# Kernel tuning notes

Hardware: AMD Instinct MI355X
Metric: run time of the kernel (lower is better)

Reference implementation:

```python
import math
import jax, jax.numpy as jnp
import numpy as np

NUM_HEADS = 16
TAU_RCS, LAMBDA_RCS = 2.0, 0.6
PATCH = 16
PREFIX = 8
GAUSS_STD = 5.0


def gaussian_window(d1, d2, std):
    c = 1.0 / (std * math.sqrt(2.0))
    k1 = (jnp.arange(d1, dtype=jnp.float32) - (d1 - 1) / 2.0) * c
    k2 = (jnp.arange(d2, dtype=jnp.float32) - (d2 - 1) / 2.0) * c
    return jnp.exp(-(k1[:, None] ** 2 + k2[None, :] ** 2))  # [d1, d2]


def attention_addition(d1, d2, prefix, std):
    # out[(a,b),(c,d)] = window[a-c+d1-1, b-d+d2-1]  (conv of delta images with window)
    win = gaussian_window(2 * d1 - 1, 2 * d2 - 1, std)
    ia = jnp.arange(d1)
    jb = jnp.arange(d2)
    r = ia[:, None] - ia[None, :] + (d1 - 1)   # [d1, d1]
    s = jb[:, None] - jb[None, :] + (d2 - 1)   # [d2, d2]
    add = win[r[:, None, :, None], s[None, :, None, :]]  # [d1,d2,d1,d2]
    add = add.reshape(d1 * d2, d1 * d2)
    add = jnp.pad(add, ((prefix, 0), (prefix, 0)))  # zero rows/cols for prefix tokens
    return add[None]  # [1, N, N]


def setup_inputs() -> dict:
    key = jax.random.key(0)
    ks = jax.random.split(key, 5)
    B, C = 4, 1024
    d1 = d2 = 512 // PATCH  # 32
    N = d1 * d2 + PREFIX    # 1032
    H = NUM_HEADS
    x = jax.random.normal(ks[0], (B, N, C), dtype=jnp.float32)
    qkv_w = jax.random.normal(ks[1], (3 * C, C), dtype=jnp.float32) * 0.02
    qkv_b = jnp.zeros((3 * C,), dtype=jnp.float32)
    proj_w = jax.random.normal(ks[2], (C, C), dtype=jnp.float32) * 0.02
    proj_b = jnp.zeros((C,), dtype=jnp.float32)
    attn_add = attention_addition(d1, d2, PREFIX, GAUSS_STD)
    # stored RCS attention maps are softmax outputs -> row-normalized positives
    rcs = jax.random.uniform(ks[3], (B * H, N, N), dtype=jnp.float32)
    rcs = rcs / jnp.sum(rcs, axis=-1, keepdims=True)
    return {"x": x, "qkv_w": qkv_w, "qkv_b": qkv_b, "proj_w": proj_w,
            "proj_b": proj_b, "attn_addition": attn_add, "rcs_attn": rcs}


def reference(x, qkv_w, qkv_b, proj_w, proj_b, attn_addition, rcs_attn):
    B, N, C = x.shape
    H = NUM_HEADS
    hd = C // H
    scale = hd ** -0.5
    qkv = jnp.einsum('bnc,dc->bnd', x, qkv_w) + qkv_b  # [B,N,3C]
    q, k, v = jnp.split(qkv, 3, axis=-1)
    def to_heads(t):
        return t.reshape(B, N, H, hd).transpose(0, 2, 1, 3).reshape(B * H, N, hd)
    k = to_heads(k)
    v = to_heads(v)
    # custom K-K attention with additive Gaussian bias
    attn = jnp.einsum('bnd,bmd->bnm', k, k) * scale + attn_addition
    attn = jax.nn.softmax(attn, axis=-1)
    # RCS blending with stored intermediate attention maps
    attn = TAU_RCS * ((1.0 - LAMBDA_RCS) * attn + LAMBDA_RCS * rcs_attn)
    out = jnp.einsum('bnm,bmd->bnd', attn, v)  # [B*H, N, hd]
    out = out.reshape(B, H, N, hd).transpose(0, 2, 1, 3).reshape(B, N, C)
    out = jnp.einsum('bnc,dc->bnd', out, proj_w) + proj_b
    return out
```

## Files before the change

kernel.cpp:

```cpp
#include <hip/hip_runtime.h>
#include <stdint.h>

#define NSEQ 1032
#define CDIM 1024
#define HD 64
#define H_HEADS 16
#define BROWS 4128
#define SCALE 0.125f

typedef __attribute__((ext_vector_type(8))) short bf16x8;
typedef __attribute__((ext_vector_type(4))) float f32x4;

__device__ __forceinline__ unsigned short f2bf(float f) {
  union { float f; uint32_t u; } c; c.f = f;
  uint32_t u = c.u;
  return (unsigned short)((u + 0x7fffu + ((u >> 16) & 1u)) >> 16);
}

__device__ __forceinline__ void gl16(const void* gp, void* lp) {
  __builtin_amdgcn_global_load_lds((const __attribute__((address_space(1))) void*)gp,
                                   (__attribute__((address_space(3))) void*)lp, 16, 0, 0);
}

__global__ void convert_f32_bf16(const float* __restrict__ src, unsigned short* __restrict__ dst, int n4) {
  int i = blockIdx.x * blockDim.x + threadIdx.x;
  if (i >= n4) return;
  float4 v = ((const float4*)src)[i];
  ushort4 o;
  o.x = f2bf(v.x); o.y = f2bf(v.y); o.z = f2bf(v.z); o.w = f2bf(v.w);
  ((ushort4*)dst)[i] = o;
}

template<int MODE>
__global__ __launch_bounds__(256, 2) void gemm_bt(
    const unsigned short* __restrict__ A,
    const unsigned short* __restrict__ Bw,
    const float* __restrict__ bias,
    unsigned short* __restrict__ outK,
    unsigned short* __restrict__ outV,
    float* __restrict__ outF,
    int M, int K)
{
  __shared__ unsigned short As[128 * 32];
  __shared__ unsigned short Bs[128 * 32];
  const int t = threadIdx.x;
  const int w = t >> 6, lane = t & 63, lr = lane & 15, lg = lane >> 4;
  const int wr = w >> 1, wc = w & 1;
  const int m0 = blockIdx.y * 128, n0 = blockIdx.x * 128;
  f32x4 acc[4][4] = {};

  for (int ks = 0; ks < K; ks += 32) {
    #pragma unroll
    for (int q = 0; q < 2; ++q) {
      const int o = t + (q << 8);
      const int row = o >> 2, kc = o & 3;
      int ra = m0 + row; ra = ra < M ? ra : M - 1;
      gl16(A + (size_t)ra * K + ks + kc * 8, (void*)(As + o * 8));
      gl16(Bw + (size_t)(n0 + row) * K + ks + kc * 8, (void*)(Bs + o * 8));
    }
    __syncthreads();
    bf16x8 af[4], bfr[4];
    #pragma unroll
    for (int m = 0; m < 4; ++m)
      af[m] = *(const bf16x8*)(As + (wr * 64 + m * 16 + lr) * 32 + lg * 8);
    #pragma unroll
    for (int n = 0; n < 4; ++n)
      bfr[n] = *(const bf16x8*)(Bs + (wc * 64 + n * 16 + lr) * 32 + lg * 8);
    #pragma unroll
    for (int m = 0; m < 4; ++m)
      #pragma unroll
      for (int n = 0; n < 4; ++n)
        acc[m][n] = __builtin_amdgcn_mfma_f32_16x16x32_bf16(af[m], bfr[n], acc[m][n], 0, 0, 0);
    __syncthreads();
  }

  #pragma unroll
  for (int m = 0; m < 4; ++m) {
    const int rowb = m0 + wr * 64 + m * 16 + lg * 4;
    #pragma unroll
    for (int n = 0; n < 4; ++n) {
      const int col = n0 + wc * 64 + n * 16 + lr;
      const float bv = bias[col];
      #pragma unroll
      for (int r = 0; r < 4; ++r) {
        const int row = rowb + r;
        if (row >= M) continue;
        const float v = acc[m][n][r] + bv;
        if (MODE == 0) {
          const int b = row / NSEQ, nn = row - b * NSEQ;
          if (col < CDIM) {
            const int h = col >> 6, d = col & 63;
            outK[((size_t)(b * H_HEADS + h) * NSEQ + nn) * HD + d] = f2bf(v);
          } else {
            const int jj = col - CDIM, h = jj >> 6, d = jj & 63;
            outV[((size_t)(b * H_HEADS + h) * HD + d) * NSEQ + nn] = f2bf(v);
          }
        } else {
          outF[(size_t)row * CDIM + col] = v;
        }
      }
    }
  }
}

__global__ __launch_bounds__(256, 2) void attn_fused(
    const unsigned short* __restrict__ Kb,
    const unsigned short* __restrict__ Vt,
    const float* __restrict__ rcs,
    unsigned short* __restrict__ outp)
{
  __shared__ __align__(16) unsigned short Kc[2][64 * 64];
  __shared__ __align__(16) unsigned short Vs[2][64 * 64];
  __shared__ __align__(16) float As[2][64 * 64];
  __shared__ unsigned short Ps[64 * 72];
  const int t = threadIdx.x;
  const int w = t >> 6, lane = t & 63, lr = lane & 15, lg = lane >> 4;
  const int bid = blockIdx.x;
  const int nb = (bid & 7) * 136 + (bid >> 3);
  const int bh = nb / 17, rt = nb - bh * 17;
  const int i_base = rt * 64 + w * 16;
  const int arow = w * 16 + lr;
  const float* rbase = rcs + (size_t)bh * NSEQ * NSEQ;
  const unsigned short* kbase = Kb + (size_t)bh * NSEQ * HD;
  const unsigned short* vbase = Vt + (size_t)bh * HD * NSEQ;

  auto stage = [&](int tile, int buf) {
    const int tB = tile * 64;
    #pragma unroll
    for (int q = 0; q < 2; ++q) {
      const int p = t + (q << 8);
      const int row = p >> 3, sch = p & 7;
      const int gch = (sch ^ row) & 7;
      int mrow = tB + row; if (mrow > NSEQ - 1) mrow = NSEQ - 1;
      gl16(kbase + (size_t)mrow * HD + gch * 8, (void*)(Kc[buf] + p * 8));
    }
    #pragma unroll
    for (int q = 0; q < 2; ++q) {
      const int p = t + (q << 8);
      const int row = p >> 3, sch = p & 7;
      const int gch = (sch ^ row) & 7;
      int gc = tB + gch * 8; if (gc > NSEQ - 8) gc = NSEQ - 8;
      gl16(vbase + (size_t)row * NSEQ + gc, (void*)(Vs[buf] + p * 8));
    }
    #pragma unroll
    for (int q = 0; q < 4; ++q) {
      const int p = t + (q << 8);
      const int row = p >> 4, sch = p & 15;
      const int gch = (sch & 8) | ((sch ^ row) & 7);
      int grow = rt * 64 + row; if (grow > NSEQ - 1) grow = NSEQ - 1;
      int gcol = tB + gch * 4; if (gcol > NSEQ - 4) gcol = NSEQ - 4;
      gl16(rbase + (size_t)grow * NSEQ + gcol, (void*)(As[buf] + p * 4));
    }
  };

  bf16x8 akr[2];
  {
    int row = i_base + lr; if (row > NSEQ - 1) row = NSEQ - 1;
    const unsigned short* p = kbase + (size_t)row * HD + lg * 8;
    akr[0] = *(const bf16x8*)(p);
    akr[1] = *(const bf16x8*)(p + 32);
  }

  const int irow_base = i_base + lg * 4;
  int i1v[4], j1v[4]; float iokf[4];
  #pragma unroll
  for (int r = 0; r < 4; ++r) {
    const int irow = irow_base + r;
    const int ip = irow - 8;
    i1v[r] = ip >> 5; j1v[r] = ip & 31;
    iokf[r] = (irow >= 8) ? 1.f : 0.f;
  }

  f32x4 accP[4] = {};
  f32x4 accR[4] = {};
  float lsum[4] = {0.f, 0.f, 0.f, 0.f};

  stage(0, 0);

  for (int mt = 0; mt < 17; ++mt) {
    const int mB = mt * 64;
    const int cur = mt & 1, nxt = cur ^ 1;

    if (mt < 16) {
      stage(mt + 1, nxt);
      asm volatile("s_waitcnt vmcnt(8)");
    } else {
      asm volatile("s_waitcnt vmcnt(0)");
    }
    __builtin_amdgcn_sched_barrier(0);
    __builtin_amdgcn_s_barrier();
    __builtin_amdgcn_sched_barrier(0);

    const unsigned short* kc = Kc[cur];
    const unsigned short* vsb = Vs[cur];

    f32x4 s[4];
    #pragma unroll
    for (int fn = 0; fn < 4; ++fn) {
      const int row = 16 * fn + lr;
      const int r7 = row & 7;
      f32x4 z = {0.f, 0.f, 0.f, 0.f};
      bf16x8 b0 = *(const bf16x8*)(kc + row * 64 + ((lg ^ r7) & 7) * 8);
      bf16x8 b1 = *(const bf16x8*)(kc + row * 64 + (((4 + lg) ^ r7) & 7) * 8);
      z = __builtin_amdgcn_mfma_f32_16x16x32_bf16(akr[0], b0, z, 0, 0, 0);
      z = __builtin_amdgcn_mfma_f32_16x16x32_bf16(akr[1], b1, z, 0, 0, 0);
      s[fn] = z;
    }

    #pragma unroll
    for (int fn = 0; fn < 4; ++fn) {
      const int mcol = mB + 16 * fn + lr;
      const int mp = mcol - 8;
      const int m1 = mp >> 5, m2 = mp & 31;
      const float mokf = (mcol >= 8 && mcol < NSEQ) ? 1.f : 0.f;
      const bool mlt = (mcol < NSEQ);
      #pragma unroll
      for (int r = 0; r < 4; ++r) {
        const int di = i1v[r] - m1, dj = j1v[r] - m2;
        const float ad = __expf(-0.02f * (float)(di * di + dj * dj)) * iokf[r] * mokf;
        const float sv = s[fn][r] * SCALE + ad;
        const float p = mlt ? __expf(sv) : 0.f;
        lsum[r] += p;
        Ps[(w * 16 + lg * 4 + r) * 72 + 16 * fn + lr] = f2bf(p);
      }
    }

    bf16x8 af[2];
    #pragma unroll
    for (int kf = 0; kf < 2; ++kf) {
      bf16x8 a;
      const int kg = mB + kf * 32 + lg * 8;
      if (kg + 8 <= NSEQ) {
        const float* ab = As[cur] + arow * 64;
        const int c0 = kf * 8 + 2 * lg;
        const int s0 = (c0 & 8) | ((c0 ^ arow) & 7);
        const int s1 = (c0 & 8) | (((c0 + 1) ^ arow) & 7);
        f32x4 lo = *(const f32x4*)(ab + s0 * 4);
        f32x4 hi = *(const f32x4*)(ab + s1 * 4);
        a[0] = (short)f2bf(lo[0]); a[1] = (short)f2bf(lo[1]);
        a[2] = (short)f2bf(lo[2]); a[3] = (short)f2bf(lo[3]);
        a[4] = (short)f2bf(hi[0]); a[5] = (short)f2bf(hi[1]);
        a[6] = (short)f2bf(hi[2]); a[7] = (short)f2bf(hi[3]);
      } else {
        #pragma unroll
        for (int j = 0; j < 8; ++j) a[j] = 0;
      }
      af[kf] = a;
    }

    bf16x8 pa0 = *(const bf16x8*)(Ps + (w * 16 + lr) * 72 + lg * 8);
    bf16x8 pa1 = *(const bf16x8*)(Ps + (w * 16 + lr) * 72 + 32 + lg * 8);
    #pragma unroll
    for (int fd = 0; fd < 4; ++fd) {
      const int row = 16 * fd + lr;
      const int r7 = row & 7;
      bf16x8 v0 = *(const bf16x8*)(vsb + row * 64 + ((lg ^ r7) & 7) * 8);
      bf16x8 v1 = *(const bf16x8*)(vsb + row * 64 + (((4 + lg) ^ r7) & 7) * 8);
      accP[fd] = __builtin_amdgcn_mfma_f32_16x16x32_bf16(pa0, v0, accP[fd], 0, 0, 0);
      accP[fd] = __builtin_amdgcn_mfma_f32_16x16x32_bf16(pa1, v1, accP[fd], 0, 0, 0);
      accR[fd] = __builtin_amdgcn_mfma_f32_16x16x32_bf16(af[0], v0, accR[fd], 0, 0, 0);
      accR[fd] = __builtin_amdgcn_mfma_f32_16x16x32_bf16(af[1], v1, accR[fd], 0, 0, 0);
    }

    __builtin_amdgcn_sched_barrier(0);
    __builtin_amdgcn_s_barrier();
    __builtin_amdgcn_sched_barrier(0);
  }

  #pragma unroll
  for (int r = 0; r < 4; ++r) {
    float v = lsum[r];
    v += __shfl_xor(v, 1); v += __shfl_xor(v, 2);
    v += __shfl_xor(v, 4); v += __shfl_xor(v, 8);
    lsum[r] = v;
  }

  const int b = bh >> 4, hh = bh & 15;
  #pragma unroll
  for (int fd = 0; fd < 4; ++fd) {
    #pragma unroll
    for (int r = 0; r < 4; ++r) {
      const int irow = i_base + lg * 4 + r;
      if (irow < NSEQ) {
        const float val = 0.8f * accP[fd][r] / lsum[r] + 1.2f * accR[fd][r];
        outp[(size_t)(b * NSEQ + irow) * CDIM + hh * 64 + 16 * fd + lr] = f2bf(val);
      }
    }
  }
}

extern "C" void kernel_launch(void* const* d_in, const int* in_sizes, int n_in,
                              void* d_out, int out_size, void* d_ws, size_t ws_size,
                              hipStream_t stream) {
  (void)in_sizes; (void)n_in; (void)out_size; (void)ws_size;
  const float* x      = (const float*)d_in[0];
  const float* qkv_w  = (const float*)d_in[1];
  const float* qkv_b  = (const float*)d_in[2];
  const float* proj_w = (const float*)d_in[3];
  const float* proj_b = (const float*)d_in[4];
  const float* rcs    = (const float*)d_in[6];
  float* out = (float*)d_out;

  char* ws = (char*)d_ws;
  unsigned short* x_bf = (unsigned short*)ws; ws += (size_t)BROWS * CDIM * 2;
  unsigned short* wkv  = (unsigned short*)ws; ws += (size_t)2048 * CDIM * 2;
  unsigned short* wp   = (unsigned short*)ws; ws += (size_t)1024 * CDIM * 2;
  unsigned short* Kb   = (unsigned short*)ws; ws += (size_t)64 * NSEQ * HD * 2;
  unsigned short* Vt   = (unsigned short*)ws; ws += (size_t)64 * HD * NSEQ * 2;
  unsigned short* op   = (unsigned short*)ws; ws += (size_t)BROWS * CDIM * 2;

  const int n1 = BROWS * CDIM / 4, n2 = 2048 * CDIM / 4, n3 = 1024 * CDIM / 4;
  convert_f32_bf16<<<(n1 + 255) / 256, 256, 0, stream>>>(x, x_bf, n1);
  convert_f32_bf16<<<(n2 + 255) / 256, 256, 0, stream>>>(qkv_w + 1024 * 1024, wkv, n2);
  convert_f32_bf16<<<(n3 + 255) / 256, 256, 0, stream>>>(proj_w, wp, n3);

  gemm_bt<0><<<dim3(16, 33), 256, 0, stream>>>(x_bf, wkv, qkv_b + 1024, Kb, Vt, nullptr, BROWS, CDIM);
  attn_fused<<<1088, 256, 0, stream>>>(Kb, Vt, rcs, op);
  gemm_bt<1><<<dim3(8, 33), 256, 0, stream>>>(op, wp, proj_b, nullptr, nullptr, out, BROWS, CDIM);
}
```

Before: 199.0 us.

## Replace per-element Gaussian exp with recurrence, precompute staging addresses, restructure barriers

Replaces the per-tile exp evaluation of the Gaussian bias with a multiplicative recurrence across m-tiles: each step multiplies u by v*C1 and v by C2, exploiting that advancing the tile by 64 columns shifts di by 2. Staging source and destination addresses are precomputed once, so non-tail tiles skip clamping arithmetic, and only the last tile keeps the clamped path. The wait-then-barrier moves to the end of each iteration, and s_setprio is raised around the MFMA blocks. Over 17 steps the recurrence can build up rounding error in the bias, and the vmcnt(0) wait at the end of each iteration may give up some of the load overlap the previous vmcnt(8) scheme allowed.

```diff
diff --git a/kernel.cpp b/kernel.cpp
--- a/kernel.cpp
+++ b/kernel.cpp
@@ -124,8 +124,36 @@
   const unsigned short* kbase = Kb + (size_t)bh * NSEQ * HD;
   const unsigned short* vbase = Vt + (size_t)bh * HD * NSEQ;
 
-  auto stage = [&](int tile, int buf) {
-    const int tB = tile * 64;
+  const unsigned short* srck[2]; int dok[2];
+  const unsigned short* srcv[2]; int dov[2];
+  const float* srca[4]; int doa[4];
+  #pragma unroll
+  for (int q = 0; q < 2; ++q) {
+    const int p = t + (q << 8);
+    const int row = p >> 3, sch = p & 7;
+    const int gch = (sch ^ row) & 7;
+    srck[q] = kbase + (size_t)row * HD + gch * 8;  dok[q] = p * 8;
+    srcv[q] = vbase + (size_t)row * NSEQ + gch * 8; dov[q] = p * 8;
+  }
+  #pragma unroll
+  for (int q = 0; q < 4; ++q) {
+    const int p = t + (q << 8);
+    const int row = p >> 4, sch = p & 15;
+    const int gch = (sch & 8) | ((sch ^ row) & 7);
+    int grow = rt * 64 + row; if (grow > NSEQ - 1) grow = NSEQ - 1;
+    srca[q] = rbase + (size_t)grow * NSEQ + gch * 4;  doa[q] = p * 4;
+  }
+
+  auto stage_fast = [&](int tB, int buf) {
+    #pragma unroll
+    for (int q = 0; q < 2; ++q) gl16(srck[q] + (size_t)tB * HD, (void*)(Kc[buf] + dok[q]));
+    #pragma unroll
+    for (int q = 0; q < 2; ++q) gl16(srcv[q] + tB, (void*)(Vs[buf] + dov[q]));
+    #pragma unroll
+    for (int q = 0; q < 4; ++q) gl16(srca[q] + tB, (void*)(As[buf] + doa[q]));
+  };
+  auto stage_tail = [&](int buf) {
+    const int tB = 1024;
     #pragma unroll
     for (int q = 0; q < 2; ++q) {
       const int p = t + (q << 8);
@@ -162,38 +190,48 @@
   }
 
   const int irow_base = i_base + lg * 4;
-  int i1v[4], j1v[4]; float iokf[4];
-  #pragma unroll
-  for (int r = 0; r < 4; ++r) {
-    const int irow = irow_base + r;
-    const int ip = irow - 8;
-    i1v[r] = ip >> 5; j1v[r] = ip & 31;
-    iokf[r] = (irow >= 8) ? 1.f : 0.f;
-  }
+  float u[16], v[16];
+  {
+    #pragma unroll
+    for (int fn = 0; fn < 4; ++fn) {
+      const int x = 16 * fn + lr;
+      const int m1_0 = ((x + 24) >> 5) - 1;
+      const int m2 = (x - 8) & 31;
+      #pragma unroll
+      for (int r = 0; r < 4; ++r) {
+        const int irow = irow_base + r;
+        const int ip = irow - 8;
+        const int i1 = ip >> 5, j1 = ip & 31;
+        const int di = i1 - m1_0, dj = j1 - m2;
+        const float iok = (irow >= 8) ? 1.f : 0.f;
+        u[fn * 4 + r] = __expf(-0.02f * (float)(di * di + dj * dj)) * iok;
+        v[fn * 4 + r] = __expf(0.08f * (float)di);
+      }
+    }
+  }
+  const float C1 = 0.92311634639f;
+  const float C2 = 0.85214378896f;
 
   f32x4 accP[4] = {};
   f32x4 accR[4] = {};
   float lsum[4] = {0.f, 0.f, 0.f, 0.f};
 
-  stage(0, 0);
+  stage_fast(0, 0);
+  asm volatile("s_waitcnt vmcnt(0)");
+  __builtin_amdgcn_s_barrier();
+  __builtin_amdgcn_sched_barrier(0);
 
   for (int mt = 0; mt < 17; ++mt) {
     const int mB = mt * 64;
     const int cur = mt & 1, nxt = cur ^ 1;
 
-    if (mt < 16) {
-      stage(mt + 1, nxt);
-      asm volatile("s_waitcnt vmcnt(8)");
-    } else {
-      asm volatile("s_waitcnt vmcnt(0)");
-    }
-    __builtin_amdgcn_sched_barrier(0);
-    __builtin_amdgcn_s_barrier();
-    __builtin_amdgcn_sched_barrier(0);
+    if (mt < 15)      stage_fast(mB + 64, nxt);
+    else if (mt == 15) stage_tail(nxt);
 
     const unsigned short* kc = Kc[cur];
     const unsigned short* vsb = Vs[cur];
 
+    __builtin_amdgcn_s_setprio(1);
     f32x4 s[4];
     #pragma unroll
     for (int fn = 0; fn < 4; ++fn) {
@@ -206,22 +244,22 @@
       z = __builtin_amdgcn_mfma_f32_16x16x32_bf16(akr[1], b1, z, 0, 0, 0);
       s[fn] = z;
     }
+    __builtin_amdgcn_s_setprio(0);
 
     #pragma unroll
     for (int fn = 0; fn < 4; ++fn) {
       const int mcol = mB + 16 * fn + lr;
-      const int mp = mcol - 8;
-      const int m1 = mp >> 5, m2 = mp & 31;
-      const float mokf = (mcol >= 8 && mcol < NSEQ) ? 1.f : 0.f;
+      const float mok = (mcol >= 8 && mcol < NSEQ) ? 1.f : 0.f;
       const bool mlt = (mcol < NSEQ);
       #pragma unroll
       for (int r = 0; r < 4; ++r) {
-        const int di = i1v[r] - m1, dj = j1v[r] - m2;
-        const float ad = __expf(-0.02f * (float)(di * di + dj * dj)) * iokf[r] * mokf;
-        const float sv = s[fn][r] * SCALE + ad;
+        const int fi = fn * 4 + r;
+        const float sv = s[fn][r] * SCALE + u[fi] * mok;
         const float p = mlt ? __expf(sv) : 0.f;
         lsum[r] += p;
         Ps[(w * 16 + lg * 4 + r) * 72 + 16 * fn + lr] = f2bf(p);
+        u[fi] *= v[fi] * C1;
+        v[fi] *= C2;
       }
     }
 
@@ -250,6 +288,7 @@
 
     bf16x8 pa0 = *(const bf16x8*)(Ps + (w * 16 + lr) * 72 + lg * 8);
     bf16x8 pa1 = *(const bf16x8*)(Ps + (w * 16 + lr) * 72 + 32 + lg * 8);
+    __builtin_amdgcn_s_setprio(1);
     #pragma unroll
     for (int fd = 0; fd < 4; ++fd) {
       const int row = 16 * fd + lr;
@@ -261,18 +300,20 @@
       accR[fd] = __builtin_amdgcn_mfma_f32_16x16x32_bf16(af[0], v0, accR[fd], 0, 0, 0);
       accR[fd] = __builtin_amdgcn_mfma_f32_16x16x32_bf16(af[1], v1, accR[fd], 0, 0, 0);
     }
+    __builtin_amdgcn_s_setprio(0);
 
     __builtin_amdgcn_sched_barrier(0);
+    asm volatile("s_waitcnt vmcnt(0)");
     __builtin_amdgcn_s_barrier();
     __builtin_amdgcn_sched_barrier(0);
   }
 
   #pragma unroll
   for (int r = 0; r < 4; ++r) {
-    float v = lsum[r];
-    v += __shfl_xor(v, 1); v += __shfl_xor(v, 2);
-    v += __shfl_xor(v, 4); v += __shfl_xor(v, 8);
-    lsum[r] = v;
+    float vv = lsum[r];
+    vv += __shfl_xor(vv, 1); vv += __shfl_xor(vv, 2);
+    vv += __shfl_xor(vv, 4); vv += __shfl_xor(vv, 8);
+    lsum[r] = vv;
   }
 
   const int b = bh >> 4, hh = bh & 15;
```

Measured after the change: 197.4 us. No clear change (-0.8%).
